# Kernel optimization log

Measured on AMD Instinct MI355X. Metric: run time of the kernel, lower is better.

## Reference

```python
import jax, jax.numpy as jnp
import numpy as np

N_NODES = 50000
N_EDGES = 800000
D_IN = 64
F1 = 64
F2 = 64
D_HID = 100


def setup_inputs() -> dict:
    key = jax.random.key(0)
    ks = jax.random.split(key, 12)
    x = jax.random.normal(ks[0], (N_NODES, D_IN), dtype=jnp.float32)
    edge_src = jax.random.randint(ks[1], (N_EDGES,), 0, N_NODES, dtype=jnp.int32)
    edge_dst = jax.random.randint(ks[2], (N_EDGES,), 0, N_NODES, dtype=jnp.int32)
    # stands in for pre-normalized GCN adjacency values (D^-1/2 (A+I) D^-1/2)
    edge_weight = jax.random.uniform(ks[3], (N_EDGES,), dtype=jnp.float32)
    def glorot(k, shape):
        lim = np.sqrt(6.0 / (shape[0] + shape[1]))
        return jax.random.uniform(k, shape, jnp.float32, -lim, lim)
    W1 = glorot(ks[4], (D_IN, F1))
    b1 = jnp.zeros((F1,), jnp.float32)
    W2 = glorot(ks[5], (F1, F2))
    b2 = jnp.zeros((F2,), jnp.float32)
    Wd = glorot(ks[6], (F2, D_HID))
    bd = jnp.zeros((D_HID,), jnp.float32)
    Wo = glorot(ks[7], (D_HID, 1))
    bo = jnp.zeros((1,), jnp.float32)
    return {"x": x, "edge_src": edge_src, "edge_dst": edge_dst,
            "edge_weight": edge_weight, "W1": W1, "b1": b1, "W2": W2,
            "b2": b2, "Wd": Wd, "bd": bd, "Wo": Wo, "bo": bo}


def _gcn_conv(x, edge_src, edge_dst, edge_weight, W, b):
    # spektral GCNConv: out = swish(A_norm @ (X @ W) + b)
    h = x @ W                                        # [N, F]
    msg = h[edge_src] * edge_weight[:, None]          # [E, F] gather + scale
    agg = jax.ops.segment_sum(msg, edge_dst, num_segments=N_NODES)  # [N, F]
    return jax.nn.swish(agg + b)


def reference(x, edge_src, edge_dst, edge_weight, W1, b1, W2, b2, Wd, bd, Wo, bo):
    h = _gcn_conv(x, edge_src, edge_dst, edge_weight, W1, b1)
    h = _gcn_conv(h, edge_src, edge_dst, edge_weight, W2, b2)
    h = jax.nn.swish(h @ Wd + bd)                    # Dense(100, swish)
    return jax.nn.sigmoid(h @ Wo + bo)               # Dense(1, sigmoid) -> [N, 1]
```

## Files before the change

### kernel.cpp

```cpp
#include <hip/hip_runtime.h>
#include <hip/hip_fp16.h>

#define N_NODES 50000
#define N_EDGES 800000
#define D 64
#define DHID 100
#define NTILES (N_NODES / 16)
#define NCT 7
#define CAP 64

typedef unsigned short ushort;
typedef unsigned int uint;
typedef __attribute__((ext_vector_type(8))) short s16x8;
typedef __attribute__((ext_vector_type(4))) float f32x4;

#define MFMA16(A, B, C) __builtin_amdgcn_mfma_f32_16x16x32_bf16((A), (B), (C), 0, 0, 0)

__device__ __forceinline__ float swishf(float x) { return x / (1.0f + __expf(-x)); }

__device__ __forceinline__ ushort f2bf(float f) {
    uint u = __float_as_uint(f);
    uint r = (u + 0x7fffu + ((u >> 16) & 1u)) >> 16;
    return (ushort)r;
}
__device__ __forceinline__ float bf2f(ushort h) { return __uint_as_float((uint)h << 16); }
__device__ __forceinline__ float bf_lo(uint d) { return __uint_as_float(d << 16); }
__device__ __forceinline__ float bf_hi(uint d) { return __uint_as_float(d & 0xffff0000u); }

__device__ __forceinline__ void accum8(float* acc, uint4 v, float w) {
    acc[0] = fmaf(w, bf_lo(v.x), acc[0]);
    acc[1] = fmaf(w, bf_hi(v.x), acc[1]);
    acc[2] = fmaf(w, bf_lo(v.y), acc[2]);
    acc[3] = fmaf(w, bf_hi(v.y), acc[3]);
    acc[4] = fmaf(w, bf_lo(v.z), acc[4]);
    acc[5] = fmaf(w, bf_hi(v.z), acc[5]);
    acc[6] = fmaf(w, bf_lo(v.w), acc[6]);
    acc[7] = fmaf(w, bf_hi(v.w), acc[7]);
}

__global__ __launch_bounds__(256) void fill_direct(const int* __restrict__ src,
                                                   const int* __restrict__ dst,
                                                   const float* __restrict__ w,
                                                   int* __restrict__ deg,
                                                   uint* __restrict__ csr) {
    int e = blockIdx.x * 256 + threadIdx.x;
    if (e < N_EDGES) {
        int d = dst[e];
        int r = atomicAdd(&deg[d], 1);
        r = min(r, CAP - 1);
        uint hw = (uint)__half_as_ushort(__float2half_rn(w[e]));
        csr[(d << 6) + r] = (uint)src[e] | (hw << 16);
    }
}

__global__ __launch_bounds__(256) void mfma_l1(const float* __restrict__ X,
                                               const float* __restrict__ W,
                                               ushort* __restrict__ H) {
    __shared__ __align__(16) short sBT[2][D][72];
    __shared__ __align__(16) short rep[4][16][72];
    int tid = threadIdx.x;
    for (int idx = tid; idx < D * D; idx += 256) {
        int k = idx >> 6, c = idx & 63;
        float wv = W[idx];
        ushort hi = f2bf(wv);
        ushort lo = f2bf(wv - bf2f(hi));
        sBT[0][c][k] = (short)hi;
        sBT[1][c][k] = (short)lo;
    }
    __syncthreads();
    int w = tid >> 6, lane = tid & 63, quad = lane >> 4, m = lane & 15;
    int tile = blockIdx.x * 4 + w;
    if (tile >= NTILES) return;
    int node0 = tile * 16;

    f32x4 acc[4] = {{0,0,0,0},{0,0,0,0},{0,0,0,0},{0,0,0,0}};
#pragma unroll
    for (int kt = 0; kt < 2; ++kt) {
        int k0 = kt * 32 + quad * 8;
        const float* xp = X + ((size_t)(node0 + m) << 6) + k0;
        float4 xa = *((const float4*)xp);
        float4 xb = *((const float4*)(xp + 4));
        float xv[8] = {xa.x, xa.y, xa.z, xa.w, xb.x, xb.y, xb.z, xb.w};
        s16x8 ahi, alo;
#pragma unroll
        for (int jj = 0; jj < 8; ++jj) {
            ushort hi = f2bf(xv[jj]);
            ahi[jj] = (short)hi;
            alo[jj] = (short)f2bf(xv[jj] - bf2f(hi));
        }
#pragma unroll
        for (int ct = 0; ct < 4; ++ct) {
            int n = ct * 16 + m;
            s16x8 bhi = *((const s16x8*)&sBT[0][n][k0]);
            s16x8 blo = *((const s16x8*)&sBT[1][n][k0]);
            acc[ct] = MFMA16(ahi, bhi, acc[ct]);
            acc[ct] = MFMA16(ahi, blo, acc[ct]);
            acc[ct] = MFMA16(alo, bhi, acc[ct]);
        }
    }
#pragma unroll
    for (int ct = 0; ct < 4; ++ct)
#pragma unroll
        for (int r = 0; r < 4; ++r)
            rep[w][quad * 4 + r][ct * 16 + m] = (short)f2bf(acc[ct][r]);
#pragma unroll
    for (int half = 0; half < 2; ++half) {
        int r = (lane >> 3) + half * 8;
        int c0 = (lane & 7) * 8;
        s16x8 v = *((const s16x8*)&rep[w][r][c0]);
        *((s16x8*)(H + ((size_t)(node0 + r) << 6) + c0)) = v;
    }
}

__global__ __launch_bounds__(256) void mfma_l2(const ushort* __restrict__ act,
                                               const float* __restrict__ W,
                                               ushort* __restrict__ H) {
    __shared__ __align__(16) short sBT[2][D][72];
    __shared__ __align__(16) short rep[4][16][72];
    int tid = threadIdx.x;
    for (int idx = tid; idx < D * D; idx += 256) {
        int k = idx >> 6, c = idx & 63;
        float wv = W[idx];
        ushort hi = f2bf(wv);
        ushort lo = f2bf(wv - bf2f(hi));
        sBT[0][c][k] = (short)hi;
        sBT[1][c][k] = (short)lo;
    }
    __syncthreads();
    int w = tid >> 6, lane = tid & 63, quad = lane >> 4, m = lane & 15;
    int tile = blockIdx.x * 4 + w;
    if (tile >= NTILES) return;
    int node0 = tile * 16;

    f32x4 acc[4] = {{0,0,0,0},{0,0,0,0},{0,0,0,0},{0,0,0,0}};
#pragma unroll
    for (int kt = 0; kt < 2; ++kt) {
        int k0 = kt * 32 + quad * 8;
        s16x8 a = *((const s16x8*)(act + ((size_t)(node0 + m) << 6) + k0));
#pragma unroll
        for (int ct = 0; ct < 4; ++ct) {
            int n = ct * 16 + m;
            s16x8 bhi = *((const s16x8*)&sBT[0][n][k0]);
            s16x8 blo = *((const s16x8*)&sBT[1][n][k0]);
            acc[ct] = MFMA16(a, bhi, acc[ct]);
            acc[ct] = MFMA16(a, blo, acc[ct]);
        }
    }
#pragma unroll
    for (int ct = 0; ct < 4; ++ct)
#pragma unroll
        for (int r = 0; r < 4; ++r)
            rep[w][quad * 4 + r][ct * 16 + m] = (short)f2bf(acc[ct][r]);
#pragma unroll
    for (int half = 0; half < 2; ++half) {
        int r = (lane >> 3) + half * 8;
        int c0 = (lane & 7) * 8;
        s16x8 v = *((const s16x8*)&rep[w][r][c0]);
        *((s16x8*)(H + ((size_t)(node0 + r) << 6) + c0)) = v;
    }
}

__global__ __launch_bounds__(256) void gather_act(const ushort* __restrict__ H,
                                                  const int* __restrict__ deg,
                                                  const uint* __restrict__ csr,
                                                  const float* __restrict__ bias,
                                                  ushort* __restrict__ actOut) {
    int tid = threadIdx.x;
    int wave = tid >> 6, lane = tid & 63;
    int j = lane >> 3, fg = lane & 7;
    int node = blockIdx.x * 4 + wave;
    int cnt = (deg[node] + 31) & ~31;
    const uint* bucket = csr + ((size_t)node << 6);

    float acc[8] = {0, 0, 0, 0, 0, 0, 0, 0};
    for (int base = 0; base < cnt; base += 32) {
        int i0 = base + j;
        uint e0 = bucket[i0];
        uint e1 = bucket[i0 + 8];
        uint e2 = bucket[i0 + 16];
        uint e3 = bucket[i0 + 24];
        float w0 = __half2float(__ushort_as_half((ushort)(e0 >> 16)));
        float w1 = __half2float(__ushort_as_half((ushort)(e1 >> 16)));
        float w2 = __half2float(__ushort_as_half((ushort)(e2 >> 16)));
        float w3 = __half2float(__ushort_as_half((ushort)(e3 >> 16)));
        uint4 v0 = *((const uint4*)(H + ((size_t)(e0 & 0xffffu) << 6) + (fg << 3)));
        uint4 v1 = *((const uint4*)(H + ((size_t)(e1 & 0xffffu) << 6) + (fg << 3)));
        uint4 v2 = *((const uint4*)(H + ((size_t)(e2 & 0xffffu) << 6) + (fg << 3)));
        uint4 v3 = *((const uint4*)(H + ((size_t)(e3 & 0xffffu) << 6) + (fg << 3)));
        accum8(acc, v0, w0);
        accum8(acc, v1, w1);
        accum8(acc, v2, w2);
        accum8(acc, v3, w3);
    }
#pragma unroll
    for (int t = 0; t < 8; ++t) {
        acc[t] += __shfl_xor(acc[t], 8, 64);
        acc[t] += __shfl_xor(acc[t], 16, 64);
        acc[t] += __shfl_xor(acc[t], 32, 64);
    }
    if (j == 0) {
        float4 ba = ((const float4*)bias)[fg * 2];
        float4 bb = ((const float4*)bias)[fg * 2 + 1];
        float r0 = swishf(acc[0] + ba.x);
        float r1 = swishf(acc[1] + ba.y);
        float r2 = swishf(acc[2] + ba.z);
        float r3 = swishf(acc[3] + ba.w);
        float r4 = swishf(acc[4] + bb.x);
        float r5 = swishf(acc[5] + bb.y);
        float r6 = swishf(acc[6] + bb.z);
        float r7 = swishf(acc[7] + bb.w);
        uint4 u;
        u.x = (uint)f2bf(r0) | ((uint)f2bf(r1) << 16);
        u.y = (uint)f2bf(r2) | ((uint)f2bf(r3) << 16);
        u.z = (uint)f2bf(r4) | ((uint)f2bf(r5) << 16);
        u.w = (uint)f2bf(r6) | ((uint)f2bf(r7) << 16);
        *((uint4*)(actOut + ((size_t)node << 6) + (fg << 3))) = u;
    }
}

__global__ __launch_bounds__(256) void mfma_head(const ushort* __restrict__ act2,
                                                 const float* __restrict__ Wd,
                                                 const float* __restrict__ bd,
                                                 const float* __restrict__ Wo,
                                                 const float* __restrict__ bo,
                                                 float* __restrict__ out) {
    __shared__ __align__(16) short sBT[2][NCT * 16][72];
    __shared__ float sbd[NCT * 16];
    __shared__ float sWo[NCT * 16];
    int tid = threadIdx.x;
    for (int idx = tid; idx < NCT * 16 * D; idx += 256) {
        int jj = idx >> 6, k = idx & 63;
        float wv = (jj < DHID) ? Wd[k * DHID + jj] : 0.f;
        ushort hi = f2bf(wv);
        ushort lo = f2bf(wv - bf2f(hi));
        sBT[0][jj][k] = (short)hi;
        sBT[1][jj][k] = (short)lo;
    }
    if (tid < NCT * 16) {
        sbd[tid] = (tid < DHID) ? bd[tid] : 0.f;
        sWo[tid] = (tid < DHID) ? Wo[tid] : 0.f;
    }
    __syncthreads();
    int w = tid >> 6, lane = tid & 63, quad = lane >> 4, m = lane & 15;
    int tile = blockIdx.x * 4 + w;
    if (tile >= NTILES) return;
    int node0 = tile * 16;

    f32x4 acc[NCT];
#pragma unroll
    for (int ct = 0; ct < NCT; ++ct) acc[ct] = (f32x4){0, 0, 0, 0};
#pragma unroll
    for (int kt = 0; kt < 2; ++kt) {
        int k0 = kt * 32 + quad * 8;
        s16x8 a = *((const s16x8*)(act2 + ((size_t)(node0 + m) << 6) + k0));
#pragma unroll
        for (int ct = 0; ct < NCT; ++ct) {
            int n = ct * 16 + m;
            s16x8 bhi = *((const s16x8*)&sBT[0][n][k0]);
            s16x8 blo = *((const s16x8*)&sBT[1][n][k0]);
            acc[ct] = MFMA16(a, bhi, acc[ct]);
            acc[ct] = MFMA16(a, blo, acc[ct]);
        }
    }
    float part[4] = {0, 0, 0, 0};
#pragma unroll
    for (int ct = 0; ct < NCT; ++ct) {
        int jj = ct * 16 + m;
        float bdv = sbd[jj], wov = sWo[jj];
#pragma unroll
        for (int r = 0; r < 4; ++r)
            part[r] = fmaf(swishf(acc[ct][r] + bdv), wov, part[r]);
    }
#pragma unroll
    for (int r = 0; r < 4; ++r) {
        part[r] += __shfl_xor(part[r], 1, 64);
        part[r] += __shfl_xor(part[r], 2, 64);
        part[r] += __shfl_xor(part[r], 4, 64);
        part[r] += __shfl_xor(part[r], 8, 64);
    }
    if (m == 0) {
        float b0 = bo[0];
        float4 o;
        o.x = 1.f / (1.f + __expf(-(part[0] + b0)));
        o.y = 1.f / (1.f + __expf(-(part[1] + b0)));
        o.z = 1.f / (1.f + __expf(-(part[2] + b0)));
        o.w = 1.f / (1.f + __expf(-(part[3] + b0)));
        *((float4*)(out + node0 + quad * 4)) = o;
    }
}

extern "C" void kernel_launch(void* const* d_in, const int* in_sizes, int n_in,
                              void* d_out, int out_size, void* d_ws, size_t ws_size,
                              hipStream_t stream) {
    const float* x   = (const float*)d_in[0];
    const int* esrc  = (const int*)d_in[1];
    const int* edst  = (const int*)d_in[2];
    const float* ew  = (const float*)d_in[3];
    const float* W1  = (const float*)d_in[4];
    const float* b1  = (const float*)d_in[5];
    const float* W2  = (const float*)d_in[6];
    const float* b2  = (const float*)d_in[7];
    const float* Wd  = (const float*)d_in[8];
    const float* bd  = (const float*)d_in[9];
    const float* Wo  = (const float*)d_in[10];
    const float* bo  = (const float*)d_in[11];
    float* out = (float*)d_out;

    char* ws = (char*)d_ws;
    ushort* H1   = (ushort*)ws;  ws += (size_t)N_NODES * D * sizeof(ushort);
    ushort* act1 = (ushort*)ws;  ws += (size_t)N_NODES * D * sizeof(ushort);
    ushort* H2   = (ushort*)ws;  ws += (size_t)N_NODES * D * sizeof(ushort);
    ushort* act2 = (ushort*)ws;  ws += (size_t)N_NODES * D * sizeof(ushort);
    uint* csr    = (uint*)ws;    ws += (size_t)N_NODES * CAP * sizeof(uint);
    int* deg     = (int*)ws;

    const int edgeBlocks = (N_EDGES + 255) / 256;
    const int mmBlocks   = (NTILES + 3) / 4;
    const int gBlocks    = N_NODES / 4;

    hipMemsetAsync(deg, 0, N_NODES * sizeof(int), stream);
    hipMemsetAsync(csr, 0, (size_t)N_NODES * CAP * sizeof(uint), stream);
    fill_direct<<<edgeBlocks, 256, 0, stream>>>(esrc, edst, ew, deg, csr);

    mfma_l1<<<mmBlocks, 256, 0, stream>>>(x, W1, H1);
    gather_act<<<gBlocks, 256, 0, stream>>>(H1, deg, csr, b1, act1);

    mfma_l2<<<mmBlocks, 256, 0, stream>>>(act1, W2, H2);
    gather_act<<<gBlocks, 256, 0, stream>>>(H2, deg, csr, b2, act2);

    mfma_head<<<mmBlocks, 256, 0, stream>>>(act2, Wd, bd, Wo, bo, out);
}
```

Baseline: 218.6 us.

## Fuse edge bucketing with layer-1 matmul and pad degree counters

Merges the edge-fill kernel and the first MFMA matmul into one launch, with block ranges split by blockIdx, so the independent work can run concurrently. Degree counters are padded to one per 64 bytes to reduce atomic contention and false sharing. The two memsets become one contiguous memset covering csr and the padded degrees. In exchange, the degree array grows 16x and the fused kernel's shared-memory allocation also applies to the fill blocks, which can lower their occupancy.

Result: no change. 215.3 us (-1.5%).

```diff
diff --git a/kernel.cpp b/kernel.cpp
--- a/kernel.cpp
+++ b/kernel.cpp
@@ -8,6 +8,8 @@
 #define NTILES (N_NODES / 16)
 #define NCT 7
 #define CAP 64
+#define FILL_BLOCKS ((N_EDGES + 255) / 256)
+#define MM_BLOCKS ((NTILES + 3) / 4)
 
 typedef unsigned short ushort;
 typedef unsigned int uint;
@@ -38,27 +40,31 @@
     acc[7] = fmaf(w, bf_hi(v.w), acc[7]);
 }
 
-__global__ __launch_bounds__(256) void fill_direct(const int* __restrict__ src,
+__global__ __launch_bounds__(256) void fill_and_l1(const int* __restrict__ src,
                                                    const int* __restrict__ dst,
                                                    const float* __restrict__ w,
-                                                   int* __restrict__ deg,
-                                                   uint* __restrict__ csr) {
-    int e = blockIdx.x * 256 + threadIdx.x;
-    if (e < N_EDGES) {
-        int d = dst[e];
-        int r = atomicAdd(&deg[d], 1);
-        r = min(r, CAP - 1);
-        uint hw = (uint)__half_as_ushort(__float2half_rn(w[e]));
-        csr[(d << 6) + r] = (uint)src[e] | (hw << 16);
-    }
-}
-
-__global__ __launch_bounds__(256) void mfma_l1(const float* __restrict__ X,
-                                               const float* __restrict__ W,
-                                               ushort* __restrict__ H) {
+                                                   int* __restrict__ degPad,
+                                                   uint* __restrict__ csr,
+                                                   const float* __restrict__ X,
+                                                   const float* __restrict__ W,
+                                                   ushort* __restrict__ H) {
     __shared__ __align__(16) short sBT[2][D][72];
     __shared__ __align__(16) short rep[4][16][72];
     int tid = threadIdx.x;
+
+    if (blockIdx.x < FILL_BLOCKS) {
+        int e = blockIdx.x * 256 + tid;
+        if (e < N_EDGES) {
+            int d = dst[e];
+            uint hw = (uint)__half_as_ushort(__float2half_rn(w[e]));
+            uint payload = (uint)src[e] | (hw << 16);
+            int r = atomicAdd(&degPad[d << 4], 1);
+            r = min(r, CAP - 1);
+            csr[(d << 6) + r] = payload;
+        }
+        return;
+    }
+
     for (int idx = tid; idx < D * D; idx += 256) {
         int k = idx >> 6, c = idx & 63;
         float wv = W[idx];
@@ -68,8 +74,8 @@
         sBT[1][c][k] = (short)lo;
     }
     __syncthreads();
-    int w = tid >> 6, lane = tid & 63, quad = lane >> 4, m = lane & 15;
-    int tile = blockIdx.x * 4 + w;
+    int wv_ = tid >> 6, lane = tid & 63, quad = lane >> 4, m = lane & 15;
+    int tile = (blockIdx.x - FILL_BLOCKS) * 4 + wv_;
     if (tile >= NTILES) return;
     int node0 = tile * 16;
 
@@ -102,12 +108,12 @@
     for (int ct = 0; ct < 4; ++ct)
 #pragma unroll
         for (int r = 0; r < 4; ++r)
-            rep[w][quad * 4 + r][ct * 16 + m] = (short)f2bf(acc[ct][r]);
+            rep[wv_][quad * 4 + r][ct * 16 + m] = (short)f2bf(acc[ct][r]);
 #pragma unroll
     for (int half = 0; half < 2; ++half) {
         int r = (lane >> 3) + half * 8;
         int c0 = (lane & 7) * 8;
-        s16x8 v = *((const s16x8*)&rep[w][r][c0]);
+        s16x8 v = *((const s16x8*)&rep[wv_][r][c0]);
         *((s16x8*)(H + ((size_t)(node0 + r) << 6) + c0)) = v;
     }
 }
@@ -161,7 +167,7 @@
 }
 
 __global__ __launch_bounds__(256) void gather_act(const ushort* __restrict__ H,
-                                                  const int* __restrict__ deg,
+                                                  const int* __restrict__ degPad,
                                                   const uint* __restrict__ csr,
                                                   const float* __restrict__ bias,
                                                   ushort* __restrict__ actOut) {
@@ -169,7 +175,7 @@
     int wave = tid >> 6, lane = tid & 63;
     int j = lane >> 3, fg = lane & 7;
     int node = blockIdx.x * 4 + wave;
-    int cnt = (deg[node] + 31) & ~31;
+    int cnt = (degPad[node << 4] + 31) & ~31;
     const uint* bucket = csr + ((size_t)node << 6);
 
     float acc[8] = {0, 0, 0, 0, 0, 0, 0, 0};
@@ -312,21 +318,19 @@
     ushort* H2   = (ushort*)ws;  ws += (size_t)N_NODES * D * sizeof(ushort);
     ushort* act2 = (ushort*)ws;  ws += (size_t)N_NODES * D * sizeof(ushort);
     uint* csr    = (uint*)ws;    ws += (size_t)N_NODES * CAP * sizeof(uint);
-    int* deg     = (int*)ws;
-
-    const int edgeBlocks = (N_EDGES + 255) / 256;
-    const int mmBlocks   = (NTILES + 3) / 4;
-    const int gBlocks    = N_NODES / 4;
-
-    hipMemsetAsync(deg, 0, N_NODES * sizeof(int), stream);
-    hipMemsetAsync(csr, 0, (size_t)N_NODES * CAP * sizeof(uint), stream);
-    fill_direct<<<edgeBlocks, 256, 0, stream>>>(esrc, edst, ew, deg, csr);
-
-    mfma_l1<<<mmBlocks, 256, 0, stream>>>(x, W1, H1);
-    gather_act<<<gBlocks, 256, 0, stream>>>(H1, deg, csr, b1, act1);
-
-    mfma_l2<<<mmBlocks, 256, 0, stream>>>(act1, W2, H2);
-    gather_act<<<gBlocks, 256, 0, stream>>>(H2, deg, csr, b2, act2);
-
-    mfma_head<<<mmBlocks, 256, 0, stream>>>(act2, Wd, bd, Wo, bo, out);
-}
+    int* degPad  = (int*)ws;     ws += (size_t)N_NODES * 16 * sizeof(int);
+
+    const int gBlocks = N_NODES / 4;
+
+    hipMemsetAsync(csr, 0, (size_t)N_NODES * (CAP + 16) * sizeof(uint), stream);
+
+    fill_and_l1<<<FILL_BLOCKS + MM_BLOCKS, 256, 0, stream>>>(esrc, edst, ew, degPad, csr,
+                                                             x, W1, H1);
+
+    gather_act<<<gBlocks, 256, 0, stream>>>(H1, degPad, csr, b1, act1);
+
+    mfma_l2<<<(NTILES + 3) / 4, 256, 0, stream>>>(act1, W2, H2);
+    gather_act<<<gBlocks, 256, 0, stream>>>(H2, degPad, csr, b2, act2);
+
+    mfma_head<<<(NTILES + 3) / 4, 256, 0, stream>>>(act2, Wd, bd, Wo, bo, out);
+}
```
